# Optimization experiments

Hardware: AMD Instinct MI355X
Metric: run time of the kernel (lower is better)

Reference implementation:

```python
import jax, jax.numpy as jnp
import numpy as np

DIM = 2048
N_HEADS = 16
N_KV_HEADS = 4
HEAD_DIM = DIM // N_HEADS  # 128
T = 2048


def setup_inputs() -> dict:
    key = jax.random.key(0)
    k1, k2, k3 = jax.random.split(key, 3)
    scale = 1.0 / np.sqrt(DIM)
    x = jax.random.normal(k1, (T, DIM), dtype=jnp.float32)
    # GQA-consistent fused QKV projection: q (n_h*hd) + k (n_kv*hd) + v (n_kv*hd)
    qkv_out = (N_HEADS + 2 * N_KV_HEADS) * HEAD_DIM  # 3072
    W_qkv = jax.random.normal(k2, (DIM, qkv_out), dtype=jnp.float32) * scale
    W_o = jax.random.normal(k3, (N_HEADS * HEAD_DIM, DIM), dtype=jnp.float32) * scale
    return {"x": x, "W_qkv": W_qkv, "W_o": W_o}


def reference(x, W_qkv, W_o):
    Tn, C = x.shape
    hd = HEAD_DIM
    qkv = x @ W_qkv  # [T, (n_h + 2*n_kv)*hd]
    q, k, v = jnp.split(qkv, [N_HEADS * hd, (N_HEADS + N_KV_HEADS) * hd], axis=-1)
    q = q.reshape(Tn, N_HEADS, hd).transpose(1, 0, 2)      # [n_h, T, hd]
    k = k.reshape(Tn, N_KV_HEADS, hd).transpose(1, 0, 2)   # [n_kv, T, hd]
    v = v.reshape(Tn, N_KV_HEADS, hd).transpose(1, 0, 2)
    rep = N_HEADS // N_KV_HEADS
    k = jnp.repeat(k, rep, axis=0)  # [n_h, T, hd]
    v = jnp.repeat(v, rep, axis=0)
    scores = jnp.einsum('hid,hjd->hij', q, k) / jnp.sqrt(jnp.asarray(hd, x.dtype))
    causal = jnp.tril(jnp.ones((Tn, Tn), dtype=bool))[None, :, :]
    scores = jnp.where(causal, scores, -jnp.inf)
    attn = jax.nn.softmax(scores, axis=-1)
    out = jnp.einsum('hij,hjd->hid', attn, v)  # [n_h, T, hd]
    out = out.transpose(1, 0, 2).reshape(Tn, N_HEADS * hd)
    return out @ W_o
```

## Files before the change

### kernel.cpp

```cpp
#include <hip/hip_runtime.h>
#include <stdint.h>

#define T_SEQ   2048
#define DMODEL  2048
#define NH      16
#define HD      128
#define QKVN    3072
#define KCOL    2048
#define VCOL    2560

typedef __bf16 bf16x8 __attribute__((ext_vector_type(8)));
typedef float  f32x4  __attribute__((ext_vector_type(4)));
typedef unsigned short u16x8 __attribute__((ext_vector_type(8)));

__device__ __forceinline__ uint16_t f2bf(float f) {
    uint32_t u = __builtin_bit_cast(uint32_t, f);
    u += 0x7fffu + ((u >> 16) & 1u);
    return (uint16_t)(u >> 16);
}
__device__ __forceinline__ float bf2f(uint16_t u) {
    return __builtin_bit_cast(float, (uint32_t)u << 16);
}
__device__ __forceinline__ u16x8 ld8(const uint16_t* p) {
    return *reinterpret_cast<const u16x8*>(p);
}
__device__ __forceinline__ void st8(uint16_t* p, u16x8 v) {
    *reinterpret_cast<u16x8*>(p) = v;
}
__device__ __forceinline__ bf16x8 as_bf(u16x8 v) { return __builtin_bit_cast(bf16x8, v); }

__device__ __forceinline__ uint32_t cvtpk(float a, float b) {
    uint32_t r;
    asm("v_cvt_pk_bf16_f32 %0, %1, %2" : "=v"(r) : "v"(a), "v"(b));
    return r;
}

__device__ __forceinline__ void gl_lds16(const uint16_t* g, uint16_t* l) {
    __builtin_amdgcn_global_load_lds((const __attribute__((address_space(1))) void*)g,
                                     (__attribute__((address_space(3))) void*)l, 16, 0, 0);
}

__global__ __launch_bounds__(256) void k_prep(const float* __restrict__ x,
                                              const float* __restrict__ Wqkv,
                                              const float* __restrict__ Wo,
                                              uint16_t* __restrict__ xb,
                                              uint16_t* __restrict__ wqt,
                                              uint16_t* __restrict__ wot) {
    __shared__ uint16_t tile[64][72];
    int b = blockIdx.x;
    int t = threadIdx.x;
    if (b < 2048) {
        int i = b * 256 + t;
        const f32x4* p = reinterpret_cast<const f32x4*>(x) + (size_t)i * 2;
        f32x4 a = p[0], c = p[1];
        u16x8 o;
        o[0] = f2bf(a[0]); o[1] = f2bf(a[1]); o[2] = f2bf(a[2]); o[3] = f2bf(a[3]);
        o[4] = f2bf(c[0]); o[5] = f2bf(c[1]); o[6] = f2bf(c[2]); o[7] = f2bf(c[3]);
        reinterpret_cast<u16x8*>(xb)[i] = o;
        return;
    }
    const float* in;
    uint16_t* out;
    int R = 2048, C, cbase, rbase;
    if (b < 3584) {
        int id = b - 2048;
        in = Wqkv; out = wqt; C = 3072;
        cbase = (id % 48) * 64; rbase = (id / 48) * 64;
    } else {
        int id = b - 3584;
        in = Wo; out = wot; C = 2048;
        cbase = (id % 32) * 64; rbase = (id / 32) * 64;
    }
#pragma unroll
    for (int p = 0; p < 4; ++p) {
        int ir = p * 16 + (t >> 4);
        int ic = (t & 15) * 4;
        f32x4 v = *reinterpret_cast<const f32x4*>(&in[(size_t)(rbase + ir) * C + cbase + ic]);
        tile[ir][ic + 0] = f2bf(v[0]);
        tile[ir][ic + 1] = f2bf(v[1]);
        tile[ir][ic + 2] = f2bf(v[2]);
        tile[ir][ic + 3] = f2bf(v[3]);
    }
    __syncthreads();
#pragma unroll
    for (int p = 0; p < 2; ++p) {
        int oc = p * 32 + (t >> 3);
        int orr = (t & 7) * 8;
        u16x8 o;
#pragma unroll
        for (int e = 0; e < 8; ++e) o[e] = tile[orr + e][oc];
        st8(&out[(size_t)(cbase + oc) * R + rbase + orr], o);
    }
}

__global__ __launch_bounds__(256) void k_gemm(const uint16_t* __restrict__ A,
                                              const uint16_t* __restrict__ Bt,
                                              void* __restrict__ Cout,
                                              uint16_t* __restrict__ vt_out,
                                              int M, int N, int K, int gy,
                                              int out_bf16, int scale_cols, float qscale) {
    __shared__ __align__(16) uint16_t Asm[2][64 * 64];
    __shared__ __align__(16) uint16_t Bsm[2][128 * 64];
    int t = threadIdx.x;
    int w = t >> 6, lane = t & 63, lo = lane & 15, g4 = lane >> 4;

    int nwg = (int)gridDim.x;
    int wg = (int)blockIdx.x;
    int idx = (wg & 7) * (nwg >> 3) + (wg >> 3);
    int bx = idx / gy, by = idx % gy;
    int mbase = by * 64, nbase = bx * 128;

    int wm = w >> 1, wn = w & 1;

    const uint16_t* pA[2]; int lofsA[2];
#pragma unroll
    for (int c = 0; c < 2; ++c) {
        int ch = w * 2 + c;
        int r = ch * 8 + (lane >> 3);
        pA[c] = A + (size_t)(mbase + r) * K + (((lane & 7) ^ (r & 7)) * 8);
        lofsA[c] = ch * 512;
    }
    const uint16_t* pB[4]; int lofsB[4];
#pragma unroll
    for (int c = 0; c < 4; ++c) {
        int ch = w * 4 + c;
        int r = ch * 8 + (lane >> 3);
        pB[c] = Bt + (size_t)(nbase + r) * K + (((lane & 7) ^ (r & 7)) * 8);
        lofsB[c] = ch * 512;
    }

    f32x4 acc[2][4] = {};

#pragma unroll
    for (int c = 0; c < 2; ++c) gl_lds16(pA[c], &Asm[0][lofsA[c]]);
#pragma unroll
    for (int c = 0; c < 4; ++c) gl_lds16(pB[c], &Bsm[0][lofsB[c]]);

    int cur = 0;
    for (int kt = 0; kt < K; kt += 64) {
        __syncthreads();
        if (kt + 64 < K) {
            int ko = kt + 64;
#pragma unroll
            for (int c = 0; c < 2; ++c) gl_lds16(pA[c] + ko, &Asm[cur ^ 1][lofsA[c]]);
#pragma unroll
            for (int c = 0; c < 4; ++c) gl_lds16(pB[c] + ko, &Bsm[cur ^ 1][lofsB[c]]);
        }
        bf16x8 af[2][2], bfr[2][4];
#pragma unroll
        for (int ks = 0; ks < 2; ++ks) {
#pragma unroll
            for (int i = 0; i < 2; ++i) {
                int ar = wm * 32 + i * 16 + lo;
                af[ks][i] = as_bf(ld8(&Asm[cur][(ar * 64 + ks * 32 + g4 * 8) ^ ((lo & 7) << 3)]));
            }
#pragma unroll
            for (int j = 0; j < 4; ++j) {
                int br = wn * 64 + j * 16 + lo;
                bfr[ks][j] = as_bf(ld8(&Bsm[cur][(br * 64 + ks * 32 + g4 * 8) ^ ((lo & 7) << 3)]));
            }
        }
        __builtin_amdgcn_s_setprio(1);
#pragma unroll
        for (int ks = 0; ks < 2; ++ks)
#pragma unroll
            for (int i = 0; i < 2; ++i)
#pragma unroll
                for (int j = 0; j < 4; ++j)
                    acc[i][j] = __builtin_amdgcn_mfma_f32_16x16x32_bf16(af[ks][i], bfr[ks][j], acc[i][j], 0, 0, 0);
        __builtin_amdgcn_s_setprio(0);
        cur ^= 1;
    }

    if (out_bf16) {
        uint16_t* C = (uint16_t*)Cout;
        bool dovt = (vt_out != nullptr) && (nbase >= VCOL);
        uint16_t* tl = &Bsm[0][0];
        if (dovt) __syncthreads();
#pragma unroll
        for (int i = 0; i < 2; ++i)
#pragma unroll
            for (int j = 0; j < 4; ++j)
#pragma unroll
                for (int r = 0; r < 4; ++r) {
                    int rowl = wm * 32 + i * 16 + g4 * 4 + r;
                    int coll = wn * 64 + j * 16 + lo;
                    int col = nbase + coll;
                    float v = acc[i][j][r];
                    if (col < scale_cols) v *= qscale;
                    uint16_t bv = f2bf(v);
                    C[(size_t)(mbase + rowl) * N + col] = bv;
                    if (dovt) tl[coll * 72 + rowl] = bv;
                }
        if (dovt) {
            __syncthreads();
            int c = t >> 1, roff = (t & 1) * 32;
            uint16_t* dst = vt_out + (size_t)(nbase - VCOL + c) * T_SEQ + mbase + roff;
            const uint16_t* srcp = &tl[c * 72 + roff];
#pragma unroll
            for (int e = 0; e < 4; ++e) st8(dst + e * 8, ld8(srcp + e * 8));
        }
    } else {
        float* C = (float*)Cout;
#pragma unroll
        for (int i = 0; i < 2; ++i)
#pragma unroll
            for (int j = 0; j < 4; ++j)
#pragma unroll
                for (int r = 0; r < 4; ++r) {
                    int row = mbase + wm * 32 + i * 16 + g4 * 4 + r;
                    int col = nbase + wn * 64 + j * 16 + lo;
                    C[(size_t)row * N + col] = acc[i][j][r];
                }
    }
}

__global__ __launch_bounds__(256) void k_attn(const uint16_t* __restrict__ qkv,
                                              const uint16_t* __restrict__ vt,
                                              uint16_t* __restrict__ po,
                                              float* __restrict__ pml) {
    __shared__ __align__(16) uint16_t Ksm[2][64 * 128];
    __shared__ __align__(16) uint16_t Vsm[2][128 * 64];
    __shared__ __align__(16) uint16_t Psm[4][16 * 72];
    int t = threadIdx.x;
    int w = t >> 6, lane = t & 63, lo = lane & 15, g4 = lane >> 4;
    int x = blockIdx.x, h = blockIdx.y, p = blockIdx.z, kh = h >> 2;

    const uint16_t* kbase = qkv + KCOL + (size_t)kh * HD;
    const uint16_t* vbase = vt + (size_t)(kh * HD) * T_SEQ;

    const uint16_t* kp[4]; const uint16_t* vp[4]; int lofs[4];
#pragma unroll
    for (int c = 0; c < 4; ++c) {
        int ch = w * 4 + c;
        int kr = ch * 4 + (lane >> 4);
        kp[c] = kbase + (size_t)kr * QKVN + ((lane & 15) ^ (kr & 7)) * 8;
        int vr = ch * 8 + (lane >> 3);
        vp[c] = vbase + (size_t)vr * T_SEQ + ((lane & 7) ^ (vr & 7)) * 8;
        lofs[c] = ch * 512;
    }

    for (int rep = 0; rep < 2; ++rep) {
        int qt = rep ? 31 - x : x;
        int qb = qt * 64;
        int cnt = (qt + 2 - p) >> 1;

        bf16x8 qf[4];
        {
            int qrow = qb + w * 16 + lo;
            const uint16_t* qp = &qkv[(size_t)qrow * QKVN + h * HD + g4 * 8];
#pragma unroll
            for (int ks = 0; ks < 4; ++ks) qf[ks] = as_bf(ld8(qp + ks * 32));
        }

        f32x4 o[8] = {};
        float mr = -INFINITY, pp = 0.f;

        if (cnt) {
            __syncthreads();
            size_t ko = (size_t)p * 64 * QKVN; int vo = p * 64;
#pragma unroll
            for (int c = 0; c < 4; ++c) {
                gl_lds16(kp[c] + ko, &Ksm[0][lofs[c]]);
                gl_lds16(vp[c] + vo, &Vsm[0][lofs[c]]);
            }
        }

        int cur = 0;
        for (int it = 0; it < cnt; ++it) {
            int jt = p + 2 * it;
            __syncthreads();
            if (it + 1 < cnt) {
                size_t ko = (size_t)(jt + 2) * 64 * QKVN;
                int vo = (jt + 2) * 64;
#pragma unroll
                for (int c = 0; c < 4; ++c) {
                    gl_lds16(kp[c] + ko, &Ksm[cur ^ 1][lofs[c]]);
                    gl_lds16(vp[c] + vo, &Vsm[cur ^ 1][lofs[c]]);
                }
            }

            f32x4 s[4] = {};
            __builtin_amdgcn_s_setprio(1);
#pragma unroll
            for (int nt = 0; nt < 4; ++nt) {
                int j = nt * 16 + lo;
#pragma unroll
                for (int ks = 0; ks < 4; ++ks) {
                    bf16x8 a = as_bf(ld8(&Ksm[cur][(j * 128 + ks * 32 + g4 * 8) ^ ((lo & 7) << 3)]));
                    s[nt] = __builtin_amdgcn_mfma_f32_16x16x32_bf16(a, qf[ks], s[nt], 0, 0, 0);
                }
            }
            __builtin_amdgcn_s_setprio(0);

            if (jt == qt) {
                int i = qb + w * 16 + lo;
                int jb = jt * 64;
#pragma unroll
                for (int nt = 0; nt < 4; ++nt)
#pragma unroll
                    for (int r = 0; r < 4; ++r) {
                        int j = jb + nt * 16 + g4 * 4 + r;
                        if (j > i) s[nt][r] = -INFINITY;
                    }
            }

            float pm = fmaxf(
                fmaxf(fmaxf(fmaxf(s[0][0], s[0][1]), fmaxf(s[0][2], s[0][3])),
                      fmaxf(fmaxf(s[1][0], s[1][1]), fmaxf(s[1][2], s[1][3]))),
                fmaxf(fmaxf(fmaxf(s[2][0], s[2][1]), fmaxf(s[2][2], s[2][3])),
                      fmaxf(fmaxf(s[3][0], s[3][1]), fmaxf(s[3][2], s[3][3]))));
            pm = fmaxf(pm, __shfl_xor(pm, 16));
            pm = fmaxf(pm, __shfl_xor(pm, 32));

            if (__any(pm > mr + 11.f)) {
                float mn = fmaxf(mr, pm);
                float al = exp2f(fminf(fmaxf(mr, -1e30f) - mn, 0.f));
                mr = mn;
                pp *= al;
                float alo[4];
#pragma unroll
                for (int r = 0; r < 4; ++r)
                    alo[r] = __shfl(al, (lane & 48) | (((lane >> 4) << 2) + r));
#pragma unroll
                for (int dt = 0; dt < 8; ++dt)
#pragma unroll
                    for (int r = 0; r < 4; ++r) o[dt][r] *= alo[r];
            }
            float msafe = fmaxf(mr, -1e30f);
#pragma unroll
            for (int nt = 0; nt < 4; ++nt)
#pragma unroll
                for (int r = 0; r < 4; ++r) {
                    float pe = exp2f(s[nt][r] - msafe);
                    s[nt][r] = pe;
                    pp += pe;
                }
#pragma unroll
            for (int nt = 0; nt < 4; ++nt) {
                uint32_t p01 = cvtpk(s[nt][0], s[nt][1]);
                uint32_t p23 = cvtpk(s[nt][2], s[nt][3]);
                *reinterpret_cast<uint2*>(&Psm[w][lo * 72 + nt * 16 + g4 * 4]) =
                    make_uint2(p01, p23);
            }

            __builtin_amdgcn_s_setprio(1);
#pragma unroll
            for (int ks2 = 0; ks2 < 2; ++ks2) {
                bf16x8 pa = as_bf(ld8(&Psm[w][lo * 72 + ks2 * 32 + g4 * 8]));
#pragma unroll
                for (int dt = 0; dt < 8; ++dt) {
                    int d = dt * 16 + lo;
                    bf16x8 vb = as_bf(ld8(&Vsm[cur][(d * 64 + ks2 * 32 + g4 * 8) ^ ((lo & 7) << 3)]));
                    o[dt] = __builtin_amdgcn_mfma_f32_16x16x32_bf16(pa, vb, o[dt], 0, 0, 0);
                }
            }
            __builtin_amdgcn_s_setprio(0);
            cur ^= 1;
        }

        float lr = pp;
        lr += __shfl_xor(lr, 16);
        lr += __shfl_xor(lr, 32);

        uint16_t* pob = po + (size_t)p * T_SEQ * DMODEL;
#pragma unroll
        for (int dt = 0; dt < 8; ++dt)
#pragma unroll
            for (int r = 0; r < 4; ++r) {
                int i = qb + w * 16 + g4 * 4 + r;
                int col = h * HD + dt * 16 + lo;
                pob[(size_t)i * DMODEL + col] = f2bf(o[dt][r]);
            }
        if (lane < 16) {
            int i = qb + w * 16 + lane;
            float* pe = pml + (size_t)p * T_SEQ * NH * 2 + ((size_t)i * NH + h) * 2;
            pe[0] = mr;
            pe[1] = lr;
        }
    }
}

__global__ __launch_bounds__(256) void k_comb(uint16_t* __restrict__ po,
                                              const float* __restrict__ pml) {
    int i = blockIdx.x * 256 + threadIdx.x;
    int row = i >> 8;
    int cg = i & 255;
    int h = cg >> 4;
    int col = cg * 8;
    const size_t PS = (size_t)T_SEQ * NH * 2;
    const size_t TD = (size_t)T_SEQ * DMODEL;
    size_t mo = ((size_t)row * NH + h) * 2;
    float m0 = pml[mo], l0 = pml[mo + 1];
    float m1 = pml[PS + mo], l1 = pml[PS + mo + 1];
    float m = fmaxf(m0, m1);
    float w0 = exp2f(m0 - m), w1 = exp2f(m1 - m);
    float rl = 1.f / (l0 * w0 + l1 * w1);
    size_t off = (size_t)row * DMODEL + col;
    u16x8 a = ld8(po + off);
    u16x8 b = ld8(po + TD + off);
    u16x8 o;
#pragma unroll
    for (int e = 0; e < 8; ++e)
        o[e] = f2bf((bf2f(a[e]) * w0 + bf2f(b[e]) * w1) * rl);
    st8(po + off, o);
}

extern "C" void kernel_launch(void* const* d_in, const int* in_sizes, int n_in,
                              void* d_out, int out_size, void* d_ws, size_t ws_size,
                              hipStream_t stream) {
    (void)in_sizes; (void)n_in; (void)out_size; (void)ws_size;
    const float* x    = (const float*)d_in[0];
    const float* Wqkv = (const float*)d_in[1];
    const float* Wo   = (const float*)d_in[2];
    float* out = (float*)d_out;

    char* ws = (char*)d_ws;
    uint16_t* xb   = (uint16_t*)(ws + 0);
    uint16_t* wqt  = (uint16_t*)(ws + 8388608);
    uint16_t* po   = (uint16_t*)(ws + 0);
    float*    pml  = (float*)(ws + 16777216);
    uint16_t* wot  = (uint16_t*)(ws + 20971520);
    uint16_t* qkvb = (uint16_t*)(ws + 29360128);
    uint16_t* vtb  = (uint16_t*)(ws + 41943040);

    const float qscale = 0.12751743f;

    k_prep<<<4608, 256, 0, stream>>>(x, Wqkv, Wo, xb, wqt, wot);
    k_gemm<<<768, 256, 0, stream>>>(xb, wqt, qkvb, vtb, 2048, 3072, 2048, 32, 1, 2048, qscale);
    k_attn<<<dim3(16, 16, 2), 256, 0, stream>>>(qkvb, vtb, po, pml);
    k_comb<<<2048, 256, 0, stream>>>(po, pml);
    k_gemm<<<512, 256, 0, stream>>>(po, wot, out, nullptr, 2048, 2048, 2048, 32, 0, 0, 1.0f);
}
```

Measured before the change: 132.2 us.

## Fuse split-KV partial combine into output projection GEMM A-tile load

Removes the separate combine kernel. The output-projection GEMM now reads both attention partials and their max/sum stats directly, merges them in registers while loading the A tile, and writes the merged bf16 values into shared memory. This avoids writing and re-reading the combined attention output and saves one kernel launch. In exchange, A loads change from async global-to-LDS copies to register loads plus exp/reciprocal math inside the GEMM main loop. The combine is also redone by every N-tile column block, about 16x redundantly.

```diff
diff --git a/kernel.cpp b/kernel.cpp
--- a/kernel.cpp
+++ b/kernel.cpp
@@ -95,10 +95,10 @@
 
 __global__ __launch_bounds__(256) void k_gemm(const uint16_t* __restrict__ A,
                                               const uint16_t* __restrict__ Bt,
-                                              void* __restrict__ Cout,
+                                              uint16_t* __restrict__ C,
                                               uint16_t* __restrict__ vt_out,
                                               int M, int N, int K, int gy,
-                                              int out_bf16, int scale_cols, float qscale) {
+                                              int scale_cols, float qscale) {
     __shared__ __align__(16) uint16_t Asm[2][64 * 64];
     __shared__ __align__(16) uint16_t Bsm[2][128 * 64];
     int t = threadIdx.x;
@@ -172,47 +172,161 @@
         cur ^= 1;
     }
 
-    if (out_bf16) {
-        uint16_t* C = (uint16_t*)Cout;
-        bool dovt = (vt_out != nullptr) && (nbase >= VCOL);
-        uint16_t* tl = &Bsm[0][0];
-        if (dovt) __syncthreads();
-#pragma unroll
-        for (int i = 0; i < 2; ++i)
-#pragma unroll
-            for (int j = 0; j < 4; ++j)
-#pragma unroll
-                for (int r = 0; r < 4; ++r) {
-                    int rowl = wm * 32 + i * 16 + g4 * 4 + r;
-                    int coll = wn * 64 + j * 16 + lo;
-                    int col = nbase + coll;
-                    float v = acc[i][j][r];
-                    if (col < scale_cols) v *= qscale;
-                    uint16_t bv = f2bf(v);
-                    C[(size_t)(mbase + rowl) * N + col] = bv;
-                    if (dovt) tl[coll * 72 + rowl] = bv;
-                }
-        if (dovt) {
-            __syncthreads();
-            int c = t >> 1, roff = (t & 1) * 32;
-            uint16_t* dst = vt_out + (size_t)(nbase - VCOL + c) * T_SEQ + mbase + roff;
-            const uint16_t* srcp = &tl[c * 72 + roff];
-#pragma unroll
-            for (int e = 0; e < 4; ++e) st8(dst + e * 8, ld8(srcp + e * 8));
-        }
-    } else {
-        float* C = (float*)Cout;
-#pragma unroll
-        for (int i = 0; i < 2; ++i)
-#pragma unroll
-            for (int j = 0; j < 4; ++j)
-#pragma unroll
-                for (int r = 0; r < 4; ++r) {
-                    int row = mbase + wm * 32 + i * 16 + g4 * 4 + r;
-                    int col = nbase + wn * 64 + j * 16 + lo;
-                    C[(size_t)row * N + col] = acc[i][j][r];
-                }
-    }
+    bool dovt = (vt_out != nullptr) && (nbase >= VCOL);
+    uint16_t* tl = &Bsm[0][0];
+    if (dovt) __syncthreads();
+#pragma unroll
+    for (int i = 0; i < 2; ++i)
+#pragma unroll
+        for (int j = 0; j < 4; ++j)
+#pragma unroll
+            for (int r = 0; r < 4; ++r) {
+                int rowl = wm * 32 + i * 16 + g4 * 4 + r;
+                int coll = wn * 64 + j * 16 + lo;
+                int col = nbase + coll;
+                float v = acc[i][j][r];
+                if (col < scale_cols) v *= qscale;
+                uint16_t bv = f2bf(v);
+                C[(size_t)(mbase + rowl) * N + col] = bv;
+                if (dovt) tl[coll * 72 + rowl] = bv;
+            }
+    if (dovt) {
+        __syncthreads();
+        int c = t >> 1, roff = (t & 1) * 32;
+        uint16_t* dst = vt_out + (size_t)(nbase - VCOL + c) * T_SEQ + mbase + roff;
+        const uint16_t* srcp = &tl[c * 72 + roff];
+#pragma unroll
+        for (int e = 0; e < 4; ++e) st8(dst + e * 8, ld8(srcp + e * 8));
+    }
+}
+
+__global__ __launch_bounds__(256) void k_gemm2(const uint16_t* __restrict__ po,
+                                               const float* __restrict__ pml,
+                                               const uint16_t* __restrict__ Bt,
+                                               float* __restrict__ C, int gy) {
+    __shared__ __align__(16) uint16_t Asm[2][64 * 64];
+    __shared__ __align__(16) uint16_t Bsm[2][128 * 64];
+    const size_t TD = (size_t)T_SEQ * DMODEL;
+    const size_t PS = (size_t)T_SEQ * NH * 2;
+    int t = threadIdx.x;
+    int w = t >> 6, lane = t & 63, lo = lane & 15, g4 = lane >> 4;
+
+    int nwg = (int)gridDim.x;
+    int wg = (int)blockIdx.x;
+    int idx = (wg & 7) * (nwg >> 3) + (wg >> 3);
+    int bx = idx / gy, by = idx % gy;
+    int mbase = by * 64, nbase = bx * 128;
+
+    int wm = w >> 1, wn = w & 1;
+
+    const uint16_t* pa0[2]; const float* pmr[2]; int lofsA[2];
+#pragma unroll
+    for (int c = 0; c < 2; ++c) {
+        int ch = w * 2 + c;
+        int r = ch * 8 + (lane >> 3);
+        int cg = ((lane & 7) ^ (r & 7)) * 8;
+        int row = mbase + r;
+        pa0[c] = po + (size_t)row * DMODEL + cg;
+        pmr[c] = pml + (size_t)row * (NH * 2);
+        lofsA[c] = ch * 512;
+    }
+    const uint16_t* pB[4]; int lofsB[4];
+#pragma unroll
+    for (int c = 0; c < 4; ++c) {
+        int ch = w * 4 + c;
+        int r = ch * 8 + (lane >> 3);
+        pB[c] = Bt + (size_t)(nbase + r) * DMODEL + (((lane & 7) ^ (r & 7)) * 8);
+        lofsB[c] = ch * 512;
+    }
+
+    f32x4 acc[2][4] = {};
+
+#pragma unroll
+    for (int c = 0; c < 4; ++c) gl_lds16(pB[c], &Bsm[0][lofsB[c]]);
+#pragma unroll
+    for (int c = 0; c < 2; ++c) {
+        u16x8 a8 = ld8(pa0[c]);
+        u16x8 b8 = ld8(pa0[c] + TD);
+        float2 ml0 = *reinterpret_cast<const float2*>(pmr[c]);
+        float2 ml1 = *reinterpret_cast<const float2*>(pmr[c] + PS);
+        float m = fmaxf(ml0.x, ml1.x);
+        float w0 = exp2f(ml0.x - m), w1 = exp2f(ml1.x - m);
+        float rl = 1.f / (ml0.y * w0 + ml1.y * w1);
+        w0 *= rl; w1 *= rl;
+        u16x8 o8;
+#pragma unroll
+        for (int e = 0; e < 8; ++e) o8[e] = f2bf(bf2f(a8[e]) * w0 + bf2f(b8[e]) * w1);
+        st8(&Asm[0][lofsA[c] + lane * 8], o8);
+    }
+
+    int cur = 0;
+    for (int kt = 0; kt < 2048; kt += 64) {
+        __syncthreads();
+        u16x8 a8[2], b8[2];
+        float2 ml0[2], ml1[2];
+        bool nx = (kt + 64 < 2048);
+        if (nx) {
+            int ko = kt + 64;
+            int h = ko >> 7;
+#pragma unroll
+            for (int c = 0; c < 4; ++c) gl_lds16(pB[c] + ko, &Bsm[cur ^ 1][lofsB[c]]);
+#pragma unroll
+            for (int c = 0; c < 2; ++c) {
+                a8[c] = ld8(pa0[c] + ko);
+                b8[c] = ld8(pa0[c] + TD + ko);
+                ml0[c] = *reinterpret_cast<const float2*>(pmr[c] + h * 2);
+                ml1[c] = *reinterpret_cast<const float2*>(pmr[c] + PS + h * 2);
+            }
+        }
+        bf16x8 af[2][2], bfr[2][4];
+#pragma unroll
+        for (int ks = 0; ks < 2; ++ks) {
+#pragma unroll
+            for (int i = 0; i < 2; ++i) {
+                int ar = wm * 32 + i * 16 + lo;
+                af[ks][i] = as_bf(ld8(&Asm[cur][(ar * 64 + ks * 32 + g4 * 8) ^ ((lo & 7) << 3)]));
+            }
+#pragma unroll
+            for (int j = 0; j < 4; ++j) {
+                int br = wn * 64 + j * 16 + lo;
+                bfr[ks][j] = as_bf(ld8(&Bsm[cur][(br * 64 + ks * 32 + g4 * 8) ^ ((lo & 7) << 3)]));
+            }
+        }
+        __builtin_amdgcn_s_setprio(1);
+#pragma unroll
+        for (int ks = 0; ks < 2; ++ks)
+#pragma unroll
+            for (int i = 0; i < 2; ++i)
+#pragma unroll
+                for (int j = 0; j < 4; ++j)
+                    acc[i][j] = __builtin_amdgcn_mfma_f32_16x16x32_bf16(af[ks][i], bfr[ks][j], acc[i][j], 0, 0, 0);
+        __builtin_amdgcn_s_setprio(0);
+        if (nx) {
+#pragma unroll
+            for (int c = 0; c < 2; ++c) {
+                float m = fmaxf(ml0[c].x, ml1[c].x);
+                float w0 = exp2f(ml0[c].x - m), w1 = exp2f(ml1[c].x - m);
+                float rl = 1.f / (ml0[c].y * w0 + ml1[c].y * w1);
+                w0 *= rl; w1 *= rl;
+                u16x8 o8;
+#pragma unroll
+                for (int e = 0; e < 8; ++e) o8[e] = f2bf(bf2f(a8[c][e]) * w0 + bf2f(b8[c][e]) * w1);
+                st8(&Asm[cur ^ 1][lofsA[c] + lane * 8], o8);
+            }
+        }
+        cur ^= 1;
+    }
+
+#pragma unroll
+    for (int i = 0; i < 2; ++i)
+#pragma unroll
+        for (int j = 0; j < 4; ++j)
+#pragma unroll
+            for (int r = 0; r < 4; ++r) {
+                int row = mbase + wm * 32 + i * 16 + g4 * 4 + r;
+                int col = nbase + wn * 64 + j * 16 + lo;
+                C[(size_t)row * DMODEL + col] = acc[i][j][r];
+            }
 }
 
 __global__ __launch_bounds__(256) void k_attn(const uint16_t* __restrict__ qkv,
@@ -381,31 +495,6 @@
     }
 }
 
-__global__ __launch_bounds__(256) void k_comb(uint16_t* __restrict__ po,
-                                              const float* __restrict__ pml) {
-    int i = blockIdx.x * 256 + threadIdx.x;
-    int row = i >> 8;
-    int cg = i & 255;
-    int h = cg >> 4;
-    int col = cg * 8;
-    const size_t PS = (size_t)T_SEQ * NH * 2;
-    const size_t TD = (size_t)T_SEQ * DMODEL;
-    size_t mo = ((size_t)row * NH + h) * 2;
-    float m0 = pml[mo], l0 = pml[mo + 1];
-    float m1 = pml[PS + mo], l1 = pml[PS + mo + 1];
-    float m = fmaxf(m0, m1);
-    float w0 = exp2f(m0 - m), w1 = exp2f(m1 - m);
-    float rl = 1.f / (l0 * w0 + l1 * w1);
-    size_t off = (size_t)row * DMODEL + col;
-    u16x8 a = ld8(po + off);
-    u16x8 b = ld8(po + TD + off);
-    u16x8 o;
-#pragma unroll
-    for (int e = 0; e < 8; ++e)
-        o[e] = f2bf((bf2f(a[e]) * w0 + bf2f(b[e]) * w1) * rl);
-    st8(po + off, o);
-}
-
 extern "C" void kernel_launch(void* const* d_in, const int* in_sizes, int n_in,
                               void* d_out, int out_size, void* d_ws, size_t ws_size,
                               hipStream_t stream) {
@@ -427,8 +516,7 @@
     const float qscale = 0.12751743f;
 
     k_prep<<<4608, 256, 0, stream>>>(x, Wqkv, Wo, xb, wqt, wot);
-    k_gemm<<<768, 256, 0, stream>>>(xb, wqt, qkvb, vtb, 2048, 3072, 2048, 32, 1, 2048, qscale);
+    k_gemm<<<768, 256, 0, stream>>>(xb, wqt, qkvb, vtb, 2048, 3072, 2048, 32, 2048, qscale);
     k_attn<<<dim3(16, 16, 2), 256, 0, stream>>>(qkvb, vtb, po, pml);
-    k_comb<<<2048, 256, 0, stream>>>(po, pml);
-    k_gemm<<<512, 256, 0, stream>>>(po, wot, out, nullptr, 2048, 2048, 2048, 32, 0, 0, 1.0f);
-}
+    k_gemm2<<<512, 256, 0, stream>>>(po, pml, wot, out, 32);
+}
```

After: 165.9 us. 1.25x slower.
